# Performance work log

Measured on AMD Instinct MI355X. Metric: run time of the kernel, lower is better.

Reference implementation:

```python
import jax, jax.numpy as jnp
import numpy as np

N_NODES = 100000
N_EDGES = 1250000
IN_CH = 128
OUT_CH = 64


def setup_inputs() -> dict:
    key = jax.random.key(0)
    k1, k2, k3, k4 = jax.random.split(key, 4)
    x = jax.random.normal(k1, (N_NODES, IN_CH), dtype=jnp.float32)
    edge_index = jax.random.randint(k2, (2, N_EDGES), 0, N_NODES, dtype=jnp.int64)
    edge_weight = jax.random.uniform(k3, (N_EDGES,), dtype=jnp.float32)
    # Xavier-uniform weight, zero bias (as in reset_parameters)
    limit = float(np.sqrt(6.0 / (IN_CH + OUT_CH)))
    W = jax.random.uniform(k4, (IN_CH, OUT_CH), dtype=jnp.float32, minval=-limit, maxval=limit)
    b = jnp.zeros((OUT_CH,), dtype=jnp.float32)
    return {"x": x, "edge_index": edge_index, "edge_weight": edge_weight, "W": W, "b": b}


def reference(x, edge_index, edge_weight, W, b):
    # Dense transform: [N, in] @ [in, out] -> [N, out]
    h = jnp.matmul(x, W)
    row, col = edge_index[0], edge_index[1]
    n = h.shape[0]
    # Weighted in-degree via scatter-add on destination (row)
    deg = jnp.zeros((n,), dtype=h.dtype).at[row].add(edge_weight)
    # deg^-0.5 with inf (deg==0) replaced by 0
    deg_inv_sqrt = jnp.where(deg == 0, jnp.zeros_like(deg), deg ** -0.5)
    norm = deg_inv_sqrt[row] * deg_inv_sqrt[col]  # [E]
    # Gather source features, normalize, scatter-add to destinations
    out = jnp.zeros_like(h).at[row].add(h[col] * norm[:, None])
    return out + b
```

## Files before the change

### kernel.cpp

```cpp
#include <hip/hip_runtime.h>

#define N_NODES 100000
#define N_EDGES 1250000
#define IN_CH 128
#define OUT_CH 64

#define NPB 128
#define ACCS2 33
#define NBINS 782
#define LSTRIDE 783
#define RECCAP 2048
#define NB1 384
#define B1T 512
#define CH1 ((N_EDGES + NB1 - 1) / NB1)
#define MAXU ((CH1 + B1T - 1) / B1T)
#define NG4 ((NBINS + 3) / 4)
#define GEMM_BLOCKS ((N_NODES + 127) / 128)

#define QSCALE 8192.0f
#define QBIAS_F 8388608.0f
#define QBIAS_U 8388608u
#define INV_QSCALE 1.220703125e-4f
#define SCALE_DEG 33554432.0f
#define INV_SCALE_DEG 2.9802322387695312e-08f

typedef __attribute__((ext_vector_type(8))) short short8;
typedef __attribute__((ext_vector_type(4))) float f32x4;

__device__ inline unsigned int f2bf(float f) {
    unsigned int u = __float_as_uint(f);
    unsigned int r = ((u >> 16) & 1u) + 0x7FFFu;
    return (u + r) >> 16;
}
__device__ inline float bf_lo(unsigned int p) { return __uint_as_float(p << 16); }
__device__ inline float bf_hi(unsigned int p) { return __uint_as_float(p & 0xFFFF0000u); }

__device__ inline unsigned long long qpacks(unsigned int p, float sc) {
    unsigned int lo = (unsigned int)__float2int_rn(fmaf(bf_lo(p), sc, QBIAS_F));
    unsigned int hi = (unsigned int)__float2int_rn(fmaf(bf_hi(p), sc, QBIAS_F));
    return ((unsigned long long)hi << 32) | (unsigned long long)lo;
}

__global__ __launch_bounds__(B1T) void sort_kernel(const int* __restrict__ ei,
                                                   const float* __restrict__ ew,
                                                   const float* __restrict__ W,
                                                   unsigned int* __restrict__ Wb,
                                                   int* __restrict__ lscan2d,
                                                   int2* __restrict__ brec) {
    __shared__ int2 srec[CH1];
    __shared__ int shist[NBINS];
    __shared__ int sscan[NBINS + 2];
    __shared__ int swsum[8];
    const int tid = threadIdx.x;

    if (blockIdx.x >= NB1) {
        int g = (blockIdx.x - NB1) * B1T + tid;
        if (g < 1024) {
            int c = g >> 8;
            int t4 = (g >> 6) & 3;
            int l = g & 63;
            int q = l >> 4, r15 = l & 15;
            unsigned int o[4];
#pragma unroll
            for (int jj = 0; jj < 4; ++jj) {
                float f0 = W[(c * 32 + q * 8 + 2 * jj)     * OUT_CH + t4 * 16 + r15];
                float f1 = W[(c * 32 + q * 8 + 2 * jj + 1) * OUT_CH + t4 * 16 + r15];
                o[jj] = f2bf(f0) | (f2bf(f1) << 16);
            }
            *(uint4*)(Wb + (size_t)g * 4) = make_uint4(o[0], o[1], o[2], o[3]);
        }
        return;
    }

    for (int i = tid; i < NBINS; i += B1T) shist[i] = 0;
    __syncthreads();

    const int e0 = blockIdx.x * CH1;
    const int total = (e0 + CH1 < N_EDGES) ? CH1 : N_EDGES - e0;

    int rowv[MAXU], colv[MAXU];
    float wv[MAXU];
#pragma unroll
    for (int u = 0; u < MAXU; ++u) {
        int e = e0 + tid + u * B1T;
        bool ok = (tid + u * B1T) < total;
        rowv[u] = ok ? ei[e] : -1;
        colv[u] = ok ? ei[N_EDGES + e] : 0;
        wv[u]   = ok ? ew[e] : 0.0f;
        if (ok) atomicAdd(&shist[rowv[u] >> 7], 1);
    }
    __syncthreads();

    const int lanev = tid & 63, wvid = tid >> 6;
    int a0 = 0, a1 = 0, a2 = 0, a3 = 0, part = 0;
    const int b0 = tid * 4;
    if (tid < 256) {
        a0 = (b0 + 0 < NBINS) ? shist[b0 + 0] : 0;
        a1 = (b0 + 1 < NBINS) ? shist[b0 + 1] : 0;
        a2 = (b0 + 2 < NBINS) ? shist[b0 + 2] : 0;
        a3 = (b0 + 3 < NBINS) ? shist[b0 + 3] : 0;
        part = a0 + a1 + a2 + a3;
    }
    int s = part;
#pragma unroll
    for (int d = 1; d < 64; d <<= 1) {
        int t2 = __shfl_up(s, d);
        if (lanev >= d) s += t2;
    }
    if (tid < 256 && lanev == 63) swsum[wvid] = s;
    __syncthreads();
    if (tid < 256) {
        int wbase = 0;
#pragma unroll
        for (int k = 0; k < 4; ++k) if (k < wvid) wbase += swsum[k];
        int base = wbase + s - part;
        if (b0 + 0 <= NBINS) sscan[b0 + 0] = base;
        if (b0 + 1 <= NBINS) sscan[b0 + 1] = base + a0;
        if (b0 + 2 <= NBINS) sscan[b0 + 2] = base + a0 + a1;
        if (b0 + 3 <= NBINS) sscan[b0 + 3] = base + a0 + a1 + a2;
    }
    __syncthreads();

    for (int i = tid; i < NBINS; i += B1T) shist[i] = 0;
    __syncthreads();

#pragma unroll
    for (int u = 0; u < MAXU; ++u) {
        if (rowv[u] >= 0) {
            int bb = rowv[u] >> 7;
            int rk = atomicAdd(&shist[bb], 1);
            srec[sscan[bb] + rk] = make_int2(((rowv[u] & 127) << 17) | colv[u],
                                             __float_as_int(wv[u]));
        }
    }
    __syncthreads();

    for (int i = tid; i < total; i += B1T) brec[e0 + i] = srec[i];
    int* lrow = lscan2d + blockIdx.x * LSTRIDE;
    for (int i = tid; i <= NBINS; i += B1T) lrow[i] = sscan[i];
}

__global__ __launch_bounds__(512) void prep_gemm_kernel(const float* __restrict__ x,
                                                        const unsigned int* __restrict__ Wb,
                                                        const int* __restrict__ lscan2d,
                                                        const int2* __restrict__ brec,
                                                        int* __restrict__ brec2,
                                                        float* __restrict__ dis,
                                                        int* __restrict__ qcnt,
                                                        int* __restrict__ mtot,
                                                        unsigned int* __restrict__ hs) {
    const int tid = threadIdx.x;

    if (blockIdx.x < NG4) {
        __shared__ int lsc[NB1][6];
        __shared__ int soff[NB1];
        __shared__ int recs[RECCAP];
        __shared__ int swsum[8];
        __shared__ unsigned long long degcnt[512];
        const int b0bin = blockIdx.x * 4;
        const int lanev = tid & 63, wvid = tid >> 6;

        degcnt[tid] = 0ull;
        if (tid < NB1) {
            const int* lrow = lscan2d + tid * LSTRIDE;
#pragma unroll
            for (int j = 0; j < 5; ++j) {
                int bi = b0bin + j;
                lsc[tid][j] = lrow[(bi < NBINS) ? bi : NBINS];
            }
        }
        __syncthreads();

        for (int j = 0; j < 4; ++j) {
            int bin = b0bin + j;
            if (bin >= NBINS) break;

            int len = (tid < NB1) ? (lsc[tid][j + 1] - lsc[tid][j]) : 0;
            int s = len;
#pragma unroll
            for (int d = 1; d < 64; d <<= 1) {
                int t2 = __shfl_up(s, d);
                if (lanev >= d) s += t2;
            }
            if (lanev == 63) swsum[wvid] = s;
            __syncthreads();
            int wbase = 0, m = 0;
#pragma unroll
            for (int k = 0; k < 8; ++k) {
                int v = swsum[k];
                if (k < wvid) wbase += v;
                m += v;
            }
            if (tid < NB1) soff[tid] = wbase + s;
            __syncthreads();

            const int mc = (m < RECCAP) ? m : RECCAP;

            for (int p = tid; p < m; p += 512) {
                int lo = 0, hi = NB1 - 1;
                while (lo < hi) {
                    int mid = (lo + hi) >> 1;
                    if (soff[mid] > p) hi = mid; else lo = mid + 1;
                }
                int excl = (lo == 0) ? 0 : soff[lo - 1];
                int2 r = brec[(size_t)lo * CH1 + lsc[lo][j] + (p - excl)];
                if (p < RECCAP) recs[p] = r.x;
                unsigned int qd =
                    (unsigned int)__float2int_rn(__int_as_float(r.y) * SCALE_DEG);
                atomicAdd(&degcnt[j * NPB + (r.x >> 17)],
                          (1ull << 32) | (unsigned long long)qd);
            }
            __syncthreads();

            for (int p = tid; p < mc; p += 512)
                brec2[(size_t)bin * RECCAP + p] = recs[p];
            if (tid == 0) mtot[bin] = mc;
            __syncthreads();
        }

        int node = b0bin * NPB + tid;
        if ((b0bin + (tid >> 7)) < NBINS && node < N_NODES) {
            unsigned long long dc = degcnt[tid];
            float d = (float)(unsigned int)dc * INV_SCALE_DEG;
            dis[node]  = (d == 0.0f) ? 0.0f : (1.0f / sqrtf(d));
            qcnt[node] = (int)(dc >> 32);
        }
    } else {
        const int blk  = blockIdx.x - NG4;
        const int w    = tid >> 6;
        const int lane = tid & 63;
        const int q    = lane >> 4, r15 = lane & 15;
        const int node = blk * 128 + w * 16 + r15;
        const int nl   = (node < N_NODES) ? node : N_NODES - 1;
        const float* xrow = x + (size_t)nl * IN_CH;

        f32x4 acc[4];
#pragma unroll
        for (int t = 0; t < 4; ++t) acc[t] = (f32x4){0.f, 0.f, 0.f, 0.f};

#pragma unroll
        for (int c = 0; c < 4; ++c) {
            float4 xa = *(const float4*)(xrow + c * 32 + q * 8);
            float4 xb = *(const float4*)(xrow + c * 32 + q * 8 + 4);
            short8 bfrag;
            bfrag[0] = (short)f2bf(xa.x); bfrag[1] = (short)f2bf(xa.y);
            bfrag[2] = (short)f2bf(xa.z); bfrag[3] = (short)f2bf(xa.w);
            bfrag[4] = (short)f2bf(xb.x); bfrag[5] = (short)f2bf(xb.y);
            bfrag[6] = (short)f2bf(xb.z); bfrag[7] = (short)f2bf(xb.w);
#pragma unroll
            for (int t = 0; t < 4; ++t) {
                short8 afrag = *(const short8*)(Wb + (size_t)((c * 4 + t) * 64 + lane) * 4);
                acc[t] = __builtin_amdgcn_mfma_f32_16x16x32_bf16(afrag, bfrag, acc[t], 0, 0, 0);
            }
        }

        if (node < N_NODES) {
#pragma unroll
            for (int t = 0; t < 4; ++t) {
                unsigned int p0 = f2bf(acc[t][0]) | (f2bf(acc[t][1]) << 16);
                unsigned int p1 = f2bf(acc[t][2]) | (f2bf(acc[t][3]) << 16);
                *(uint2*)(hs + (size_t)node * 32 + t * 8 + q * 2) = make_uint2(p0, p1);
            }
        }
    }
}

__global__ __launch_bounds__(256) void gather_kernel(const int* __restrict__ mtot,
                                                     const int* __restrict__ brec2,
                                                     const uint4* __restrict__ hs,
                                                     const float* __restrict__ dis,
                                                     const int* __restrict__ qcnt,
                                                     const float* __restrict__ b,
                                                     float* __restrict__ out) {
    __shared__ unsigned long long acc[64 * ACCS2];
    const int tid  = threadIdx.x;
    const int blk  = blockIdx.x >> 1;
    const int half = blockIdx.x & 1;
    for (int k = tid; k < 64 * ACCS2; k += 256) acc[k] = 0ull;
    __syncthreads();

    const int m = mtot[blk];
    const int rbase = blk * RECCAP;
    const int grp = tid >> 3, l8 = tid & 7;

    for (int p0 = grp * 4; p0 < m; p0 += 128) {
        bool ok[4];
        int rec[4];
        uint4 h[4];
        float sc[4];
#pragma unroll
        for (int s = 0; s < 4; ++s) {
            int pp = p0 + s;
            int r = (pp < m) ? brec2[rbase + pp] : 0;
            rec[s] = r;
            ok[s] = (pp < m) && (((r >> 23) & 1) == half);
        }
#pragma unroll
        for (int s = 0; s < 4; ++s) {
            int col = rec[s] & 0x1FFFF;
            h[s]  = ok[s] ? hs[(size_t)col * 8 + l8] : make_uint4(0, 0, 0, 0);
            sc[s] = ok[s] ? QSCALE * dis[col] : 0.0f;
        }
#pragma unroll
        for (int s = 0; s < 4; ++s) {
            if (ok[s]) {
                int ba = ((rec[s] >> 17) & 63) * ACCS2 + 4 * l8;
                atomicAdd(&acc[ba + 0], qpacks(h[s].x, sc[s]));
                atomicAdd(&acc[ba + 1], qpacks(h[s].y, sc[s]));
                atomicAdd(&acc[ba + 2], qpacks(h[s].z, sc[s]));
                atomicAdd(&acc[ba + 3], qpacks(h[s].w, sc[s]));
            }
        }
    }
    __syncthreads();

    const unsigned int* acc32 = (const unsigned int*)acc;
    const int wid = tid >> 6, lane = tid & 63;
    float bc = b[lane];
    int chalf = lane & 1, slot = lane >> 1;
#pragma unroll 4
    for (int r = 0; r < 16; ++r) {
        int rl = wid * 16 + r;
        int node = blk * NPB + half * 64 + rl;
        if (node < N_NODES) {
            unsigned int raw = acc32[(rl * ACCS2 + slot) * 2 + chalf];
            int qsum = (int)(raw - (unsigned int)qcnt[node] * QBIAS_U);
            float di = dis[node] * INV_QSCALE;
            out[(size_t)node * OUT_CH + lane] = (float)qsum * di + bc;
        }
    }
}

extern "C" void kernel_launch(void* const* d_in, const int* in_sizes, int n_in,
                              void* d_out, int out_size, void* d_ws, size_t ws_size,
                              hipStream_t stream) {
    const float* x  = (const float*)d_in[0];
    const int*   ei = (const int*)d_in[1];
    const float* ew = (const float*)d_in[2];
    const float* W  = (const float*)d_in[3];
    const float* b  = (const float*)d_in[4];
    float* out = (float*)d_out;

    unsigned int* hs = (unsigned int*)d_ws;
    unsigned int* Wb = hs + (size_t)N_NODES * 32;
    int* lscan2d = (int*)(Wb + 4096);
    int* mtot    = lscan2d + (size_t)NB1 * LSTRIDE;
    float* dis   = (float*)(mtot + 800);
    int* qcnt    = (int*)(dis + N_NODES);
    int* brec2   = qcnt + N_NODES;
    int2* brec   = (int2*)(brec2 + (size_t)NBINS * RECCAP);
    (void)ws_size; (void)in_sizes; (void)n_in; (void)out_size;

    sort_kernel<<<NB1 + 2, B1T, 0, stream>>>(ei, ew, W, Wb, lscan2d, brec);
    prep_gemm_kernel<<<NG4 + GEMM_BLOCKS, 512, 0, stream>>>(x, Wb, lscan2d, brec,
                                                            brec2, dis, qcnt,
                                                            mtot, hs);
    gather_kernel<<<NBINS * 2, 256, 0, stream>>>(mtot, brec2, (const uint4*)hs,
                                                 dis, qcnt, b, out);
}
```

Before: 171.3 us.

## Split gather work by output channel halves instead of destination node halves

The gather kernel's two blocks per bin now each cover all 128 destination nodes but only half of the 64 output channels, rather than half the nodes and all channels. Each block processes every edge record of the bin with no node-half filtering, loading 8-byte slices of the source features and issuing two LDS atomics per record instead of four. The intent is to remove the wasted record reads and branch divergence from records rejected by the node-half test, and to balance work between the two blocks. In exchange, every block reads the full record list and dis values, and the feature gathers become narrower per lane.

```diff
diff --git a/kernel.cpp b/kernel.cpp
--- a/kernel.cpp
+++ b/kernel.cpp
@@ -6,7 +6,7 @@
 #define OUT_CH 64
 
 #define NPB 128
-#define ACCS2 33
+#define ACCH 17
 #define NBINS 782
 #define LSTRIDE 783
 #define RECCAP 2048
@@ -267,66 +267,65 @@
 
 __global__ __launch_bounds__(256) void gather_kernel(const int* __restrict__ mtot,
                                                      const int* __restrict__ brec2,
-                                                     const uint4* __restrict__ hs,
+                                                     const unsigned int* __restrict__ hs,
                                                      const float* __restrict__ dis,
                                                      const int* __restrict__ qcnt,
                                                      const float* __restrict__ b,
                                                      float* __restrict__ out) {
-    __shared__ unsigned long long acc[64 * ACCS2];
+    __shared__ unsigned long long acc[NPB * ACCH];
     const int tid  = threadIdx.x;
     const int blk  = blockIdx.x >> 1;
     const int half = blockIdx.x & 1;
-    for (int k = tid; k < 64 * ACCS2; k += 256) acc[k] = 0ull;
+    for (int k = tid; k < NPB * ACCH; k += 256) acc[k] = 0ull;
     __syncthreads();
 
     const int m = mtot[blk];
     const int rbase = blk * RECCAP;
     const int grp = tid >> 3, l8 = tid & 7;
-
-    for (int p0 = grp * 4; p0 < m; p0 += 128) {
-        bool ok[4];
-        int rec[4];
-        uint4 h[4];
-        float sc[4];
-#pragma unroll
-        for (int s = 0; s < 4; ++s) {
+    const int hoff = half * 16 + l8 * 2;
+
+    for (int p0 = grp * 8; p0 < m; p0 += 256) {
+        bool ok[8];
+        int rec[8];
+        uint2 h[8];
+        float sc[8];
+#pragma unroll
+        for (int s = 0; s < 8; ++s) {
             int pp = p0 + s;
-            int r = (pp < m) ? brec2[rbase + pp] : 0;
-            rec[s] = r;
-            ok[s] = (pp < m) && (((r >> 23) & 1) == half);
-        }
-#pragma unroll
-        for (int s = 0; s < 4; ++s) {
+            ok[s] = pp < m;
+            rec[s] = ok[s] ? brec2[rbase + pp] : 0;
+        }
+#pragma unroll
+        for (int s = 0; s < 8; ++s) {
             int col = rec[s] & 0x1FFFF;
-            h[s]  = ok[s] ? hs[(size_t)col * 8 + l8] : make_uint4(0, 0, 0, 0);
+            h[s]  = ok[s] ? *(const uint2*)(hs + (size_t)col * 32 + hoff)
+                          : make_uint2(0, 0);
             sc[s] = ok[s] ? QSCALE * dis[col] : 0.0f;
         }
 #pragma unroll
-        for (int s = 0; s < 4; ++s) {
+        for (int s = 0; s < 8; ++s) {
             if (ok[s]) {
-                int ba = ((rec[s] >> 17) & 63) * ACCS2 + 4 * l8;
+                int ba = (rec[s] >> 17) * ACCH + 2 * l8;
                 atomicAdd(&acc[ba + 0], qpacks(h[s].x, sc[s]));
                 atomicAdd(&acc[ba + 1], qpacks(h[s].y, sc[s]));
-                atomicAdd(&acc[ba + 2], qpacks(h[s].z, sc[s]));
-                atomicAdd(&acc[ba + 3], qpacks(h[s].w, sc[s]));
             }
         }
     }
     __syncthreads();
 
     const unsigned int* acc32 = (const unsigned int*)acc;
-    const int wid = tid >> 6, lane = tid & 63;
-    float bc = b[lane];
-    int chalf = lane & 1, slot = lane >> 1;
+    const int lc = tid & 31;
+    const int sl = lc >> 1, hw = lc & 1;
+    float bc = b[half * 32 + lc];
 #pragma unroll 4
     for (int r = 0; r < 16; ++r) {
-        int rl = wid * 16 + r;
-        int node = blk * NPB + half * 64 + rl;
+        int nl = (tid >> 5) + 8 * r;
+        int node = blk * NPB + nl;
         if (node < N_NODES) {
-            unsigned int raw = acc32[(rl * ACCS2 + slot) * 2 + chalf];
+            unsigned int raw = acc32[(nl * ACCH + sl) * 2 + hw];
             int qsum = (int)(raw - (unsigned int)qcnt[node] * QBIAS_U);
             float di = dis[node] * INV_QSCALE;
-            out[(size_t)node * OUT_CH + lane] = (float)qsum * di + bc;
+            out[(size_t)node * OUT_CH + half * 32 + lc] = (float)qsum * di + bc;
         }
     }
 }
@@ -355,6 +354,6 @@
     prep_gemm_kernel<<<NG4 + GEMM_BLOCKS, 512, 0, stream>>>(x, Wb, lscan2d, brec,
                                                             brec2, dis, qcnt,
                                                             mtot, hs);
-    gather_kernel<<<NBINS * 2, 256, 0, stream>>>(mtot, brec2, (const uint4*)hs,
+    gather_kernel<<<NBINS * 2, 256, 0, stream>>>(mtot, brec2, hs,
                                                  dis, qcnt, b, out);
 }
```

New measurement: 177.2 us. +3.4%, slower.
